# Kernel optimization log

Measured on AMD Instinct MI355X. Metric: run time of the kernel, lower is better.

## Reference

```python
import jax, jax.numpy as jnp
import numpy as np

DIM = 1024; DEPTH = 6; HEADS = 16; DH = 64; NF = 16; VOCAB = 20000; B = 4; N = 1024
INNER = HEADS * DH
FF_INNER = int(DIM * 4 * 2 / 3)  # GEGLU inner dim = 2730


def _ln(x, g):
    # torch F.layer_norm with beta=0 buffer, eps=1e-5
    m = x.mean(-1, keepdims=True)
    v = ((x - m) ** 2).mean(-1, keepdims=True)
    return (x - m) / jnp.sqrt(v + 1e-5) * g


def _attn(x, ctx, mask, ln_g, Wq, Wkv, Wo):
    # faithful: LayerNorm applied to x (queries); context, if given, used raw for k/v
    xn = _ln(x, ln_g)
    kv_x = xn if ctx is None else ctx
    b, i, _ = x.shape
    j = kv_x.shape[1]
    q = (xn @ Wq).reshape(b, i, HEADS, DH) * (DH ** -0.5)
    k, v = jnp.split(kv_x @ Wkv, 2, axis=-1)
    k = k.reshape(b, j, HEADS, DH)
    v = v.reshape(b, j, HEADS, DH)
    sim = jnp.einsum('bihd,bjhd->bhij', q, k)
    sim = jnp.where(mask, sim, -jnp.finfo(sim.dtype).max)
    attn = jax.nn.softmax(sim, axis=-1)
    out = jnp.einsum('bhij,bjhd->bihd', attn, v).reshape(b, i, INNER)
    return out @ Wo


def _closs(a, b, ls):
    # CLIP-style ContrastiveLossWithTemperature
    an = a / jnp.linalg.norm(a, axis=-1, keepdims=True)
    bn = b / jnp.linalg.norm(b, axis=-1, keepdims=True)
    logits = jnp.exp(ls) * (an @ bn.T)
    lab = jnp.arange(a.shape[0])
    la = -jax.nn.log_softmax(logits, axis=-1)[lab, lab].mean()
    lb = -jax.nn.log_softmax(logits.T, axis=-1)[lab, lab].mean()
    return (la + lb) * 0.5


def setup_inputs() -> dict:
    key = jax.random.key(0)
    ks = jax.random.split(key, 16)
    rn = lambda k, s: jax.random.normal(k, s, jnp.float32) * 0.02
    return {
        'spliced_data': jax.random.normal(ks[0], (B, N), jnp.float32),
        'spliced_index': jax.random.randint(ks[1], (B, N), 0, VOCAB),
        'emb': rn(ks[2], (VOCAB, DIM)),
        'fusion_tokens': jax.random.normal(ks[3], (NF, DIM), jnp.float32),
        'return_tokens': jax.random.normal(ks[4], (2, DIM), jnp.float32),
        'ln1_g': jnp.ones((DEPTH, DIM), jnp.float32),
        'Wq': rn(ks[5], (DEPTH, DIM, INNER)),
        'Wkv': rn(ks[6], (DEPTH, DIM, 2 * INNER)),
        'Wo': rn(ks[7], (DEPTH, INNER, DIM)),
        'ln2_g': jnp.ones((DEPTH, DIM), jnp.float32),
        'Wff1': rn(ks[8], (DEPTH, DIM, 2 * FF_INNER)),
        'Wff2': rn(ks[9], (DEPTH, FF_INNER, DIM)),
        'norm_g': jnp.ones((DIM,), jnp.float32),
        'pool_ln_g': jnp.ones((DIM,), jnp.float32),
        'pWq': rn(ks[10], (DIM, INNER)),
        'pWkv': rn(ks[11], (DIM, 2 * INNER)),
        'pWo': rn(ks[12], (INNER, DIM)),
        'logit_scale_c': jnp.float32(np.log(1.0 / 0.07)),
        'logit_scale_f': jnp.float32(np.log(1.0 / 0.07)),
    }


def reference(spliced_data, spliced_index, emb, fusion_tokens, return_tokens,
              ln1_g, Wq, Wkv, Wo, ln2_g, Wff1, Wff2, norm_g,
              pool_ln_g, pWq, pWkv, pWo, logit_scale_c, logit_scale_f):
    b = spliced_data.shape[0]
    # BioZorroEncoder: value-weighted embedding lookup
    spliced_tokens = emb[spliced_index] * spliced_data[..., None]  # [b, N, DIM]
    tokens = jnp.concatenate(
        [spliced_tokens, jnp.broadcast_to(fusion_tokens, (b, NF, DIM))], axis=1)
    tt = jnp.concatenate([jnp.zeros((N,), jnp.int32), jnp.ones((NF,), jnp.int32)])
    # spliced attends spliced; fusion attends everything
    zmask = (tt[:, None] == tt[None, :]) | (tt[:, None] == 1)

    def body(t, p):
        l1, wq, wkv, wo, l2, w1, w2 = p
        t = _attn(t, None, zmask, l1, wq, wkv, wo) + t
        h = _ln(t, l2) @ w1
        xh, gate = jnp.split(h, 2, axis=-1)
        t = (jax.nn.gelu(gate, approximate=False) * xh) @ w2 + t
        return t, None

    tokens, _ = jax.lax.scan(body, tokens, (ln1_g, Wq, Wkv, Wo, ln2_g, Wff1, Wff2))
    tokens = _ln(tokens, norm_g)

    rtt = jnp.array([0, 1], jnp.int32)
    pm0 = rtt[:, None] == tt[None, :]
    # faithful to source operator precedence: (pm0 | rtt) == GLOBAL(2) -> all False
    pm = (pm0.astype(jnp.int32) | rtt[:, None]) == 2

    ret = jnp.broadcast_to(return_tokens, (b, 2, DIM))
    pooled = _attn(ret, tokens, pm, pool_ln_g, pWq, pWkv, pWo) + ret

    spliced = pooled[:, 0]
    fusion = pooled[:, 1]
    loss = _closs(spliced, spliced, logit_scale_c) + _closs(spliced, fusion, logit_scale_f)
    return loss
```

## Files before the change

### kernel.cpp

```cpp
#include <hip/hip_runtime.h>

typedef unsigned short u16;
typedef unsigned long long u64;
typedef __attribute__((ext_vector_type(8))) short short8;
typedef __attribute__((ext_vector_type(4))) float f32x4;

__device__ __forceinline__ u16 f2b(float f) {
  union { float f; unsigned u; } x; x.f = f;
  unsigned r = x.u + 0x7fffu + ((x.u >> 16) & 1u);
  return (u16)(r >> 16);
}
__device__ __forceinline__ float b2f(u16 h) {
  union { unsigned u; float f; } x; x.u = ((unsigned)h) << 16;
  return x.f;
}
__device__ __forceinline__ void gld16(const void* g, void* l) {
  __builtin_amdgcn_global_load_lds(
      (__attribute__((address_space(1))) const void*)g,
      (__attribute__((address_space(3))) void*)l, 16, 0, 0);
}

__global__ __launch_bounds__(256) void embed_k(
    const float* __restrict__ data, const int* __restrict__ idx,
    const float* __restrict__ emb, const float* __restrict__ fus,
    float* __restrict__ t) {
  int row = blockIdx.x;
  int b = row / 1040, n = row % 1040;
  int tid = threadIdx.x;
  const float4* src;
  float sc = 1.f;
  if (n < 1024) {
    int e = idx[b * 1024 + n];
    sc = data[b * 1024 + n];
    src = (const float4*)(emb + (long)e * 1024);
  } else {
    src = (const float4*)(fus + (long)(n - 1024) * 1024);
  }
  float4 v = src[tid];
  v.x *= sc; v.y *= sc; v.z *= sc; v.w *= sc;
  ((float4*)(t + (long)row * 1024))[tid] = v;
}

__global__ __launch_bounds__(256) void wtrans5_k(
    const float* __restrict__ sWq, const float* __restrict__ sWkv,
    const float* __restrict__ sWo, const float* __restrict__ sW1,
    const float* __restrict__ sW2,
    u16* __restrict__ dQkvT, u16* __restrict__ dWoT,
    u16* __restrict__ dF1T, u16* __restrict__ dF2T) {
  int id = blockIdx.x;
  const float* src; u16* dst; int K, N, Kpad, nx; float sc = 1.f;
  if (id < 1024)       { src = sWq;  dst = dQkvT;             K = 1024; N = 1024; Kpad = 1024; nx = 32; sc = 0.125f; }
  else if (id < 3072)  { id -= 1024; src = sWkv; dst = dQkvT + 1024 * 1024; K = 1024; N = 2048; Kpad = 1024; nx = 64; }
  else if (id < 4096)  { id -= 3072; src = sWo;  dst = dWoT;  K = 1024; N = 1024; Kpad = 1024; nx = 32; }
  else if (id < 9600)  { id -= 4096; src = sW1;  dst = dF1T;  K = 1024; N = 5460; Kpad = 1024; nx = 172; }
  else                 { id -= 9600; src = sW2;  dst = dF2T;  K = 2730; N = 1024; Kpad = 2752; nx = 32; }
  int n0 = (id % nx) * 32, k0 = (id / nx) * 32;
  __shared__ float tile[32][33];
  int x = threadIdx.x & 31, y = threadIdx.x >> 5;
#pragma unroll
  for (int i = 0; i < 4; i++) {
    int k = k0 + y + i * 8, n = n0 + x;
    tile[y + i * 8][x] = (k < K && n < N) ? src[(long)k * N + n] * sc : 0.f;
  }
  __syncthreads();
#pragma unroll
  for (int i = 0; i < 4; i++) {
    int n = n0 + y + i * 8, k = k0 + x;
    dst[(long)n * Kpad + k] = f2b(tile[x][y + i * 8]);
  }
}

__global__ __launch_bounds__(256) void ln_k(
    const float* __restrict__ t, const float* __restrict__ g,
    u16* __restrict__ xn) {
  int row = blockIdx.x, tid = threadIdx.x;
  int wave = tid >> 6, lane = tid & 63;
  float4 v = ((const float4*)(t + (long)row * 1024))[tid];
  float s = v.x + v.y + v.z + v.w;
#pragma unroll
  for (int o = 32; o > 0; o >>= 1) s += __shfl_xor(s, o, 64);
  __shared__ float r1[4], r2[4];
  if (lane == 0) r1[wave] = s;
  __syncthreads();
  float mean = (r1[0] + r1[1] + r1[2] + r1[3]) * (1.f / 1024.f);
  float dx = v.x - mean, dy = v.y - mean, dz = v.z - mean, dw = v.w - mean;
  float q = dx * dx + dy * dy + dz * dz + dw * dw;
#pragma unroll
  for (int o = 32; o > 0; o >>= 1) q += __shfl_xor(q, o, 64);
  if (lane == 0) r2[wave] = q;
  __syncthreads();
  float var = (r2[0] + r2[1] + r2[2] + r2[3]) * (1.f / 1024.f);
  float inv = rsqrtf(var + 1e-5f);
  float4 gv = ((const float4*)g)[tid];
  u64 pack = (u64)f2b(dx * inv * gv.x)
           | ((u64)f2b(dy * inv * gv.y) << 16)
           | ((u64)f2b(dz * inv * gv.z) << 32)
           | ((u64)f2b(dw * inv * gv.w) << 48);
  *(u64*)(xn + (long)row * 1024 + tid * 4) = pack;
}

__global__ __launch_bounds__(256) void lnred_k(
    float* __restrict__ t, const float* __restrict__ p0, const float* __restrict__ p1,
    const float* __restrict__ g, u16* __restrict__ xn) {
  int row = blockIdx.x, tid = threadIdx.x;
  int wave = tid >> 6, lane = tid & 63;
  long base = (long)row * 1024;
  float4 v = ((const float4*)(t + base))[tid];
  float4 a = ((const float4*)(p0 + base))[tid];
  float4 bq = ((const float4*)(p1 + base))[tid];
  v.x += a.x + bq.x; v.y += a.y + bq.y; v.z += a.z + bq.z; v.w += a.w + bq.w;
  ((float4*)(t + base))[tid] = v;
  float s = v.x + v.y + v.z + v.w;
#pragma unroll
  for (int o = 32; o > 0; o >>= 1) s += __shfl_xor(s, o, 64);
  __shared__ float r1[4], r2[4];
  if (lane == 0) r1[wave] = s;
  __syncthreads();
  float mean = (r1[0] + r1[1] + r1[2] + r1[3]) * (1.f / 1024.f);
  float dx = v.x - mean, dy = v.y - mean, dz = v.z - mean, dw = v.w - mean;
  float q = dx * dx + dy * dy + dz * dz + dw * dw;
#pragma unroll
  for (int o = 32; o > 0; o >>= 1) q += __shfl_xor(q, o, 64);
  if (lane == 0) r2[wave] = q;
  __syncthreads();
  float var = (r2[0] + r2[1] + r2[2] + r2[3]) * (1.f / 1024.f);
  float inv = rsqrtf(var + 1e-5f);
  float4 gv = ((const float4*)g)[tid];
  u64 pack = (u64)f2b(dx * inv * gv.x)
           | ((u64)f2b(dy * inv * gv.y) << 16)
           | ((u64)f2b(dz * inv * gv.z) << 32)
           | ((u64)f2b(dw * inv * gv.w) << 48);
  *(u64*)(xn + base + tid * 4) = pack;
}

__global__ __launch_bounds__(256) void redrow_k(
    float* __restrict__ t, const float* __restrict__ p0, const float* __restrict__ p1,
    float* __restrict__ rowm, float* __restrict__ rinv) {
  int row = blockIdx.x, tid = threadIdx.x;
  int wave = tid >> 6, lane = tid & 63;
  long base = (long)row * 1024;
  float4 v = ((const float4*)(t + base))[tid];
  float4 a = ((const float4*)(p0 + base))[tid];
  float4 bq = ((const float4*)(p1 + base))[tid];
  v.x += a.x + bq.x; v.y += a.y + bq.y; v.z += a.z + bq.z; v.w += a.w + bq.w;
  ((float4*)(t + base))[tid] = v;
  float s = v.x + v.y + v.z + v.w;
#pragma unroll
  for (int o = 32; o > 0; o >>= 1) s += __shfl_xor(s, o, 64);
  __shared__ float r1[4], r2[4];
  if (lane == 0) r1[wave] = s;
  __syncthreads();
  float mean = (r1[0] + r1[1] + r1[2] + r1[3]) * (1.f / 1024.f);
  float dx = v.x - mean, dy = v.y - mean, dz = v.z - mean, dw = v.w - mean;
  float q = dx * dx + dy * dy + dz * dz + dw * dw;
#pragma unroll
  for (int o = 32; o > 0; o >>= 1) q += __shfl_xor(q, o, 64);
  if (lane == 0) r2[wave] = q;
  __syncthreads();
  if (tid == 0) {
    float var = (r2[0] + r2[1] + r2[2] + r2[3]) * (1.f / 1024.f);
    rowm[row] = mean;
    rinv[row] = rsqrtf(var + 1e-5f);
  }
}

__global__ __launch_bounds__(256) void gemm_bt(
    const u16* __restrict__ A, int lda,
    const u16* __restrict__ Bt, int ldb,
    void* __restrict__ C, int ldc,
    int K, int mode, int gx, int ns, long pstride) {
  __shared__ u16 As[3][128 * 32];
  __shared__ u16 Bs[3][128 * 32];
  int tid = threadIdx.x;
  int wave = tid >> 6, lane = tid & 63;
  int col = lane & 15, grp = lane >> 4;
  int nwg = gridDim.x;
  int id = blockIdx.x;
  int q = nwg >> 3, r = nwg & 7;
  int xcd = id & 7, off = id >> 3;
  int wgid = (xcd < r ? xcd * (q + 1) : r * (q + 1) + (xcd - r) * q) + off;
  int tiles = nwg / ns;
  int ksp = wgid / tiles;
  int rem = wgid % tiles;
  int bm = rem % gx, bn = rem / gx;
  int nst = K >> 5;
  int k0 = ((nst * ksp) / ns) << 5;
  int k1 = ((nst * (ksp + 1)) / ns) << 5;
  int sr = wave * 16 + (lane >> 2);
  int sk = ((lane & 3) ^ ((lane >> 3) & 3)) * 8;
  const u16* aSrc = A + ((long)bm * 128 + sr) * lda + sk;
  const u16* bSrc = Bt + ((long)bn * 128 + sr) * ldb + sk;
  int wm = (wave >> 1) * 64, wn = (wave & 1) * 64;
  f32x4 acc[4][4] = {};

#define GSTAGE(buf, kt) do { \
    _Pragma("unroll") \
    for (int qq = 0; qq < 2; qq++) { \
      gld16(aSrc + (kt) + (long)qq * 64 * lda, &As[buf][wave * 512 + qq * 2048]); \
      gld16(bSrc + (kt) + (long)qq * 64 * ldb, &Bs[buf][wave * 512 + qq * 2048]); \
    } } while (0)

  GSTAGE(0, k0);
  if (k0 + 32 < k1) GSTAGE(1, k0 + 32);
  int cur = 0;
  int slot = (grp ^ ((col >> 1) & 3)) * 8;
  for (int kt = k0; kt < k1; kt += 32) {
    if (kt + 64 < k1) {
      int nb = cur + 2; if (nb >= 3) nb -= 3;
      GSTAGE(nb, kt + 64);
      asm volatile("s_waitcnt vmcnt(8)" ::: "memory");
    } else if (kt + 32 < k1) {
      asm volatile("s_waitcnt vmcnt(4)" ::: "memory");
    } else {
      asm volatile("s_waitcnt vmcnt(0)" ::: "memory");
    }
    __builtin_amdgcn_s_barrier();
    __builtin_amdgcn_sched_barrier(0);
    short8 af[4], bfv[4];
#pragma unroll
    for (int m = 0; m < 4; m++)
      af[m] = *(const short8*)&As[cur][(wm + m * 16 + col) * 32 + slot];
#pragma unroll
    for (int n = 0; n < 4; n++)
      bfv[n] = *(const short8*)&Bs[cur][(wn + n * 16 + col) * 32 + slot];
    __builtin_amdgcn_s_setprio(1);
#pragma unroll
    for (int m = 0; m < 4; m++)
#pragma unroll
      for (int n = 0; n < 4; n++)
        acc[m][n] = __builtin_amdgcn_mfma_f32_16x16x32_bf16(af[m], bfv[n], acc[m][n], 0, 0, 0);
    __builtin_amdgcn_s_setprio(0);
    __builtin_amdgcn_s_barrier();
    __builtin_amdgcn_sched_barrier(0);
    cur = (cur == 2) ? 0 : cur + 1;
  }
#undef GSTAGE
  long r0 = (long)bm * 128 + wm + grp * 4;
  int c0 = bn * 128 + wn + col;
  if (mode == 0) {
    u16* Cb = (u16*)C;
#pragma unroll
    for (int m = 0; m < 4; m++)
#pragma unroll
      for (int n = 0; n < 4; n++)
#pragma unroll
        for (int rr = 0; rr < 4; rr++)
          Cb[(r0 + m * 16 + rr) * ldc + c0 + n * 16] = f2b(acc[m][n][rr]);
  } else {
    float* Cf = (float*)C + (long)ksp * pstride;
#pragma unroll
    for (int m = 0; m < 4; m++)
#pragma unroll
      for (int n = 0; n < 4; n++)
#pragma unroll
        for (int rr = 0; rr < 4; rr++)
          Cf[(r0 + m * 16 + rr) * ldc + c0 + n * 16] = acc[m][n][rr];
  }
}

__global__ __launch_bounds__(256) void vtrans_k(
    const u16* __restrict__ qkv, u16* __restrict__ vt) {
  int bh = blockIdx.x, jt = blockIdx.y;
  int b = bh >> 4, h = bh & 15;
  __shared__ u16 tile[64][65];
  int x = threadIdx.x & 63, y = threadIdx.x >> 6;
#pragma unroll
  for (int r = 0; r < 16; r++) {
    int jl = r * 4 + y;
    int j = jt * 64 + jl;
    u16 val = 0;
    if (j < 1040) val = qkv[((long)b * 1040 + j) * 3072 + 2048 + h * 64 + x];
    tile[jl][x] = val;
  }
  __syncthreads();
  long ob = (long)bh * 64 * 1040;
#pragma unroll
  for (int r = 0; r < 16; r++) {
    int d = r * 4 + y;
    int j = jt * 64 + x;
    if (j < 1040) vt[ob + (long)d * 1040 + j] = tile[x][d];
  }
}

__global__ __launch_bounds__(256) void attn_k(
    const u16* __restrict__ qkv, const u16* __restrict__ vt,
    u16* __restrict__ out) {
  int bh = blockIdx.x, it = blockIdx.y;
  int b = bh >> 4, h = bh & 15;
  int tid = threadIdx.x, wave = tid >> 6, lane = tid & 63;
  int col = lane & 15, grp = lane >> 4;
  int i0 = it * 64;
  int jmax = (it == 16) ? 1040 : 1024;
  const u16* qb = qkv + (long)b * 1040 * 3072 + h * 64;
  const u16* kb = qkv + (long)b * 1040 * 3072 + 1024 + h * 64;
  const u16* vb = vt + (long)bh * 64 * 1040;
  __shared__ u16 Ks[2][64 * 64];
  __shared__ u16 Vs[2][64 * 64];
  __shared__ u16 Ps[4][16 * 64];

  int srow0 = wave * 8 + (lane >> 3);
  int gsw = ((lane & 7) ^ (srow0 & 7)) * 8;
#define ASTAGE(buf, j0s) do { \
    _Pragma("unroll") \
    for (int qq = 0; qq < 2; qq++) { \
      int rr = qq * 32 + srow0; \
      gld16(kb + (long)((j0s) + rr) * 3072 + gsw, &Ks[buf][qq * 2048 + wave * 512]); \
      gld16(vb + (long)rr * 1040 + (j0s) + gsw, &Vs[buf][qq * 2048 + wave * 512]); \
    } } while (0)

  short8 aq[2];
  int qrow = i0 + wave * 16;
#pragma unroll
  for (int kf = 0; kf < 2; kf++)
    aq[kf] = *(const short8*)(qb + (long)(qrow + col) * 3072 + kf * 32 + grp * 8);

  f32x4 oa[4] = {};
  float lrow[4] = {0.f, 0.f, 0.f, 0.f};

  ASTAGE(0, 0);
  int cur = 0;
  for (int j0 = 0; j0 < jmax; j0 += 64) {
    if (j0 + 64 < jmax) {
      ASTAGE(cur ^ 1, j0 + 64);
      asm volatile("s_waitcnt vmcnt(4)" ::: "memory");
    } else {
      asm volatile("s_waitcnt vmcnt(0)" ::: "memory");
    }
    __builtin_amdgcn_s_barrier();
    __builtin_amdgcn_sched_barrier(0);
    f32x4 s[4] = {};
#pragma unroll
    for (int kf = 0; kf < 2; kf++) {
      short8 bk[4];
#pragma unroll
      for (int n = 0; n < 4; n++) {
        int rk = n * 16 + col;
        bk[n] = *(const short8*)&Ks[cur][rk * 64 + ((kf * 32 + grp * 8) ^ ((rk & 7) << 3))];
      }
      __builtin_amdgcn_s_setprio(1);
#pragma unroll
      for (int n = 0; n < 4; n++)
        s[n] = __builtin_amdgcn_mfma_f32_16x16x32_bf16(aq[kf], bk[n], s[n], 0, 0, 0);
      __builtin_amdgcn_s_setprio(0);
    }
    if (j0 + 64 > jmax) {
      int lim = jmax - j0;
#pragma unroll
      for (int n = 0; n < 4; n++) {
        if (n * 16 + col >= lim) {
#pragma unroll
          for (int r = 0; r < 4; r++) s[n][r] = -1e30f;
        }
      }
    }
#pragma unroll
    for (int r = 0; r < 4; r++) {
      int rp = grp * 4 + r;
      float rs = 0.f;
#pragma unroll
      for (int n = 0; n < 4; n++) {
        float p = __expf(s[n][r]);
        rs += p;
        Ps[wave][rp * 64 + ((n * 16 + col) ^ ((rp & 7) << 3))] = f2b(p);
      }
#pragma unroll
      for (int o = 1; o < 16; o <<= 1) rs += __shfl_xor(rs, o, 64);
      lrow[r] += rs;
    }
#pragma unroll
    for (int kf = 0; kf < 2; kf++) {
      short8 ap, bv[4];
      int rm = col;
      ap = *(const short8*)&Ps[wave][rm * 64 + ((kf * 32 + grp * 8) ^ ((rm & 7) << 3))];
#pragma unroll
      for (int n = 0; n < 4; n++) {
        int rv = n * 16 + col;
        bv[n] = *(const short8*)&Vs[cur][rv * 64 + ((kf * 32 + grp * 8) ^ ((rv & 7) << 3))];
      }
      __builtin_amdgcn_s_setprio(1);
#pragma unroll
      for (int n = 0; n < 4; n++)
        oa[n] = __builtin_amdgcn_mfma_f32_16x16x32_bf16(ap, bv[n], oa[n], 0, 0, 0);
      __builtin_amdgcn_s_setprio(0);
    }
    __builtin_amdgcn_s_barrier();
    __builtin_amdgcn_sched_barrier(0);
    cur ^= 1;
  }
#undef ASTAGE
#pragma unroll
  for (int n = 0; n < 4; n++)
#pragma unroll
    for (int r = 0; r < 4; r++) {
      int i = i0 + wave * 16 + grp * 4 + r;
      if (i < 1040)
        out[((long)b * 1040 + i) * 1024 + h * 64 + n * 16 + col] = f2b(oa[n][r] / lrow[r]);
    }
}

__global__ __launch_bounds__(256) void act_k(
    const u16* __restrict__ h, u16* __restrict__ act) {
  int row = blockIdx.x;
  int c = blockIdx.y * 1024 + threadIdx.x * 4;
  if (c >= 2752) return;
  const u16* hr = h + (long)row * 5504;
  u64 pack = 0;
#pragma unroll
  for (int i = 0; i < 4; i++) {
    int cc = c + i;
    float r = 0.f;
    if (cc < 2730) {
      float xh = b2f(hr[cc]);
      float gt = b2f(hr[2730 + cc]);
      float ge = 0.5f * gt * (1.f + erff(gt * 0.70710678118f));
      r = ge * xh;
    }
    pack |= ((u64)f2b(r)) << (16 * i);
  }
  *(u64*)(act + (long)row * 2752 + c) = pack;
}

__global__ __launch_bounds__(256) void wcolsum_k(
    const float* __restrict__ t, const float* __restrict__ rowm,
    const float* __restrict__ rinv, float* __restrict__ colsum,
    float* __restrict__ msum) {
  int b = blockIdx.x, c = blockIdx.y, tid = threadIdx.x;
  float a0 = 0, a1 = 0, a2 = 0, a3 = 0, ms = 0;
  for (int r = 0; r < 20; r++) {
    long row = (long)b * 1040 + c * 20 + r;
    float iv = rinv[row];
    float4 v = ((const float4*)(t + row * 1024))[tid];
    a0 += v.x * iv; a1 += v.y * iv; a2 += v.z * iv; a3 += v.w * iv;
    if (tid == 0) ms += rowm[row] * iv;
  }
  atomicAdd(&colsum[b * 1024 + tid * 4 + 0], a0);
  atomicAdd(&colsum[b * 1024 + tid * 4 + 1], a1);
  atomicAdd(&colsum[b * 1024 + tid * 4 + 2], a2);
  atomicAdd(&colsum[b * 1024 + tid * 4 + 3], a3);
  if (tid == 0) atomicAdd(&msum[b], ms);
}

__global__ __launch_bounds__(256) void mv1_k(
    const float* __restrict__ colsum, const float* __restrict__ msum,
    const float* __restrict__ g, const float* __restrict__ pWkv,
    float* __restrict__ tmp) {
  int b = blockIdx.x, n = blockIdx.y * 256 + threadIdx.x;
  float msb = msum[b];
  float acc = 0.f;
  for (int k = 0; k < 1024; k++) {
    float mk = g[k] * (colsum[b * 1024 + k] - msb);
    acc += mk * pWkv[(long)k * 2048 + 1024 + n];
  }
  tmp[b * 1024 + n] = acc * (1.f / 1040.f);
}

__global__ __launch_bounds__(256) void mv2_k(
    const float* __restrict__ tmp, const float* __restrict__ pWo,
    const float* __restrict__ ret, float* __restrict__ spl,
    float* __restrict__ fub) {
  int b = blockIdx.x, n = blockIdx.y * 256 + threadIdx.x;
  float acc = 0.f;
  for (int k = 0; k < 1024; k++) acc += tmp[b * 1024 + k] * pWo[(long)k * 1024 + n];
  spl[b * 1024 + n] = ret[n] + acc;
  fub[b * 1024 + n] = ret[1024 + n] + acc;
}

__device__ float closs_dev(const float L[4][4]) {
  float la = 0.f, lb = 0.f;
  for (int i = 0; i < 4; i++) {
    float mx = fmaxf(fmaxf(L[i][0], L[i][1]), fmaxf(L[i][2], L[i][3]));
    float sm = expf(L[i][0] - mx) + expf(L[i][1] - mx) + expf(L[i][2] - mx) + expf(L[i][3] - mx);
    la += mx + logf(sm) - L[i][i];
  }
  for (int j = 0; j < 4; j++) {
    float mx = fmaxf(fmaxf(L[0][j], L[1][j]), fmaxf(L[2][j], L[3][j]));
    float sm = expf(L[0][j] - mx) + expf(L[1][j] - mx) + expf(L[2][j] - mx) + expf(L[3][j] - mx);
    lb += mx + logf(sm) - L[j][j];
  }
  return 0.125f * (la + lb);
}

__global__ __launch_bounds__(256) void loss_k(
    const float* __restrict__ s, const float* __restrict__ f,
    const float* __restrict__ lsc, const float* __restrict__ lsf,
    float* __restrict__ out) {
  __shared__ float dots[36];
  int tid = threadIdx.x, wave = tid >> 6, lane = tid & 63;
  for (int d = wave; d < 36; d += 4) {
    const float *a, *bb;
    if (d < 16) { a = s + (d >> 2) * 1024; bb = s + (d & 3) * 1024; }
    else if (d < 32) { int e = d - 16; a = s + (e >> 2) * 1024; bb = f + (e & 3) * 1024; }
    else { a = f + (d - 32) * 1024; bb = a; }
    float p = 0.f;
    for (int k = lane; k < 1024; k += 64) p += a[k] * bb[k];
#pragma unroll
    for (int o = 32; o > 0; o >>= 1) p += __shfl_xor(p, o, 64);
    if (lane == 0) dots[d] = p;
  }
  __syncthreads();
  if (tid == 0) {
    float nS[4], nF[4];
    for (int i = 0; i < 4; i++) { nS[i] = sqrtf(dots[i * 4 + i]); nF[i] = sqrtf(dots[32 + i]); }
    float e1 = expf(lsc[0]), e2 = expf(lsf[0]);
    float L1[4][4], L2[4][4];
    for (int i = 0; i < 4; i++)
      for (int j = 0; j < 4; j++) {
        L1[i][j] = e1 * dots[i * 4 + j] / (nS[i] * nS[j]);
        L2[i][j] = e2 * dots[16 + i * 4 + j] / (nS[i] * nF[j]);
      }
    out[0] = closs_dev(L1) + closs_dev(L2);
  }
}

extern "C" void kernel_launch(void* const* d_in, const int* in_sizes, int n_in,
                              void* d_out, int out_size, void* d_ws, size_t ws_size,
                              hipStream_t stream) {
  (void)in_sizes; (void)n_in; (void)out_size; (void)ws_size;
  const float* sdata = (const float*)d_in[0];
  const int*   sidx  = (const int*)d_in[1];
  const float* emb   = (const float*)d_in[2];
  const float* fus   = (const float*)d_in[3];
  const float* ret   = (const float*)d_in[4];
  const float* ln1g  = (const float*)d_in[5];
  const float* Wq    = (const float*)d_in[6];
  const float* Wkv   = (const float*)d_in[7];
  const float* Wo    = (const float*)d_in[8];
  const float* ln2g  = (const float*)d_in[9];
  const float* Wff1  = (const float*)d_in[10];
  const float* Wff2  = (const float*)d_in[11];
  const float* normg = (const float*)d_in[12];
  const float* pWkv  = (const float*)d_in[15];
  const float* pWo   = (const float*)d_in[16];
  const float* lsc   = (const float*)d_in[17];
  const float* lsf   = (const float*)d_in[18];

  char* ws = (char*)d_ws;
  float* t   = (float*)(ws + 0L);
  u16* xn    = (u16*)(ws + 17301504L);
  char* U    = ws + 25952256L;
  u16* qkv   = (u16*)(U);
  u16* vtb   = (u16*)(U + 26738688L);
  u16* aout  = (u16*)(U + 35270656L);
  u16* hb    = (u16*)(U);
  u16* ab    = (u16*)(U + 46497792L);
  float* par0 = (float*)(U);
  float* par1 = (float*)(U + 17301504L);
  char* WT   = ws + 95698944L;
  u16* qkvT  = (u16*)(WT);
  u16* WoT   = (u16*)(WT + 6291456L);
  u16* f1T   = (u16*)(WT + 8388608L);
  u16* f2T   = (u16*)(WT + 19660800L);
  char* FIN  = ws + 120995840L;
  float* rowm   = (float*)(FIN);
  float* rinvp  = (float*)(FIN + 16640L);
  float* colsum = (float*)(FIN + 33280L);
  float* msum   = (float*)(FIN + 49664L);
  float* tmp    = (float*)(FIN + 49728L);
  float* spl    = (float*)(FIN + 66112L);
  float* fub    = (float*)(FIN + 82496L);
  const long PSTR = 4224L * 1024;

  embed_k<<<4160, 256, 0, stream>>>(sdata, sidx, emb, fus, t);

  for (int l = 0; l < 6; l++) {
    wtrans5_k<<<12352, 256, 0, stream>>>(
        Wq + (long)l * 1024 * 1024, Wkv + (long)l * 1024 * 2048,
        Wo + (long)l * 1024 * 1024, Wff1 + (long)l * 1024 * 5460,
        Wff2 + (long)l * 2730 * 1024, qkvT, WoT, f1T, f2T);

    if (l == 0)
      ln_k<<<4160, 256, 0, stream>>>(t, ln1g, xn);
    else
      lnred_k<<<4160, 256, 0, stream>>>(t, par0, par1, ln1g + l * 1024, xn);

    gemm_bt<<<33 * 24, 256, 0, stream>>>(xn, 1024, qkvT, 1024, qkv, 3072, 1024, 0, 33, 1, 0);
    vtrans_k<<<dim3(64, 17), 256, 0, stream>>>(qkv, vtb);
    attn_k<<<dim3(64, 17), 256, 0, stream>>>(qkv, vtb, aout);
    gemm_bt<<<33 * 8 * 2, 256, 0, stream>>>(aout, 1024, WoT, 1024, par0, 1024, 1024, 1, 33, 2, PSTR);
    lnred_k<<<4160, 256, 0, stream>>>(t, par0, par1, ln2g + l * 1024, xn);
    gemm_bt<<<33 * 43, 256, 0, stream>>>(xn, 1024, f1T, 1024, hb, 5504, 1024, 0, 33, 1, 0);
    act_k<<<dim3(4160, 3), 256, 0, stream>>>(hb, ab);
    gemm_bt<<<33 * 8 * 2, 256, 0, stream>>>(ab, 2752, f2T, 2752, par0, 1024, 2752, 1, 33, 2, PSTR);
  }

  redrow_k<<<4160, 256, 0, stream>>>(t, par0, par1, rowm, rinvp);
  hipMemsetAsync(colsum, 0, 16448, stream);
  wcolsum_k<<<dim3(4, 52), 256, 0, stream>>>(t, rowm, rinvp, colsum, msum);
  mv1_k<<<dim3(4, 4), 256, 0, stream>>>(colsum, msum, normg, pWkv, tmp);
  mv2_k<<<dim3(4, 4), 256, 0, stream>>>(tmp, pWo, ret, spl, fub);
  loss_k<<<1, 256, 0, stream>>>(spl, fub, lsc, lsf, (float*)d_out);
}
```

Baseline: 2.074 ms.

## Fuse V transpose into QKV GEMM epilogue and compute softmax row sums via MFMA

The QKV GEMM gains a mode that, for V-column tiles, also writes the transposed V layout straight from the accumulators, so the separate vtrans kernel launch and its extra read and write of V go away. The attention kernel clamps V tile loads at the sequence end, because the padded region is no longer zero-filled. It also computes the softmax row sums with an extra MFMA against a ones vector, dropping the per-row shuffle reductions. The risks are strided 8-byte scattered stores in the GEMM epilogue, and row sums now taken from bf16-rounded probabilities.

```diff
diff --git a/kernel.cpp b/kernel.cpp
--- a/kernel.cpp
+++ b/kernel.cpp
@@ -168,7 +168,7 @@
     const u16* __restrict__ A, int lda,
     const u16* __restrict__ Bt, int ldb,
     void* __restrict__ C, int ldc,
-    int K, int mode, int gx, int ns, long pstride) {
+    int K, int mode, int gx, int ns, long pstride, u16* __restrict__ vt) {
   __shared__ u16 As[3][128 * 32];
   __shared__ u16 Bs[3][128 * 32];
   int tid = threadIdx.x;
@@ -237,7 +237,7 @@
 #undef GSTAGE
   long r0 = (long)bm * 128 + wm + grp * 4;
   int c0 = bn * 128 + wn + col;
-  if (mode == 0) {
+  if (mode != 1) {
     u16* Cb = (u16*)C;
 #pragma unroll
     for (int m = 0; m < 4; m++)
@@ -246,6 +246,25 @@
 #pragma unroll
         for (int rr = 0; rr < 4; rr++)
           Cb[(r0 + m * 16 + rr) * ldc + c0 + n * 16] = f2b(acc[m][n][rr]);
+    if (mode == 2 && bn >= 16) {
+#pragma unroll
+      for (int m = 0; m < 4; m++) {
+        long row = r0 + m * 16;
+        if (row < 4160) {
+          int bidx = (int)(row / 1040);
+          int j = (int)(row - (long)bidx * 1040);
+#pragma unroll
+          for (int n = 0; n < 4; n++) {
+            int d = c0 + n * 16 - 2048;
+            u64 pack = (u64)f2b(acc[m][n][0])
+                     | ((u64)f2b(acc[m][n][1]) << 16)
+                     | ((u64)f2b(acc[m][n][2]) << 32)
+                     | ((u64)f2b(acc[m][n][3]) << 48);
+            *(u64*)(vt + ((long)(bidx * 16 + (d >> 6)) * 64 + (d & 63)) * 1040 + j) = pack;
+          }
+        }
+      }
+    }
   } else {
     float* Cf = (float*)C + (long)ksp * pstride;
 #pragma unroll
@@ -255,30 +274,6 @@
 #pragma unroll
         for (int rr = 0; rr < 4; rr++)
           Cf[(r0 + m * 16 + rr) * ldc + c0 + n * 16] = acc[m][n][rr];
-  }
-}
-
-__global__ __launch_bounds__(256) void vtrans_k(
-    const u16* __restrict__ qkv, u16* __restrict__ vt) {
-  int bh = blockIdx.x, jt = blockIdx.y;
-  int b = bh >> 4, h = bh & 15;
-  __shared__ u16 tile[64][65];
-  int x = threadIdx.x & 63, y = threadIdx.x >> 6;
-#pragma unroll
-  for (int r = 0; r < 16; r++) {
-    int jl = r * 4 + y;
-    int j = jt * 64 + jl;
-    u16 val = 0;
-    if (j < 1040) val = qkv[((long)b * 1040 + j) * 3072 + 2048 + h * 64 + x];
-    tile[jl][x] = val;
-  }
-  __syncthreads();
-  long ob = (long)bh * 64 * 1040;
-#pragma unroll
-  for (int r = 0; r < 16; r++) {
-    int d = r * 4 + y;
-    int j = jt * 64 + x;
-    if (j < 1040) vt[ob + (long)d * 1040 + j] = tile[x][d];
   }
 }
 
@@ -301,11 +296,12 @@
   int srow0 = wave * 8 + (lane >> 3);
   int gsw = ((lane & 7) ^ (srow0 & 7)) * 8;
 #define ASTAGE(buf, j0s) do { \
+    int jv = (j0s) + gsw; if (jv >= 1040) jv = 1032; \
     _Pragma("unroll") \
     for (int qq = 0; qq < 2; qq++) { \
       int rr = qq * 32 + srow0; \
       gld16(kb + (long)((j0s) + rr) * 3072 + gsw, &Ks[buf][qq * 2048 + wave * 512]); \
-      gld16(vb + (long)rr * 1040 + (j0s) + gsw, &Vs[buf][qq * 2048 + wave * 512]); \
+      gld16(vb + (long)rr * 1040 + jv, &Vs[buf][qq * 2048 + wave * 512]); \
     } } while (0)
 
   short8 aq[2];
@@ -314,8 +310,14 @@
   for (int kf = 0; kf < 2; kf++)
     aq[kf] = *(const short8*)(qb + (long)(qrow + col) * 3072 + kf * 32 + grp * 8);
 
+  short8 one8 = {};
+  if (col == 0) {
+#pragma unroll
+    for (int i = 0; i < 8; i++) one8[i] = (short)0x3F80;
+  }
+
   f32x4 oa[4] = {};
-  float lrow[4] = {0.f, 0.f, 0.f, 0.f};
+  f32x4 oa1 = {};
 
   ASTAGE(0, 0);
   int cur = 0;
@@ -356,16 +358,11 @@
 #pragma unroll
     for (int r = 0; r < 4; r++) {
       int rp = grp * 4 + r;
-      float rs = 0.f;
 #pragma unroll
       for (int n = 0; n < 4; n++) {
         float p = __expf(s[n][r]);
-        rs += p;
         Ps[wave][rp * 64 + ((n * 16 + col) ^ ((rp & 7) << 3))] = f2b(p);
       }
-#pragma unroll
-      for (int o = 1; o < 16; o <<= 1) rs += __shfl_xor(rs, o, 64);
-      lrow[r] += rs;
     }
 #pragma unroll
     for (int kf = 0; kf < 2; kf++) {
@@ -381,6 +378,7 @@
 #pragma unroll
       for (int n = 0; n < 4; n++)
         oa[n] = __builtin_amdgcn_mfma_f32_16x16x32_bf16(ap, bv[n], oa[n], 0, 0, 0);
+      oa1 = __builtin_amdgcn_mfma_f32_16x16x32_bf16(ap, one8, oa1, 0, 0, 0);
       __builtin_amdgcn_s_setprio(0);
     }
     __builtin_amdgcn_s_barrier();
@@ -388,13 +386,16 @@
     cur ^= 1;
   }
 #undef ASTAGE
+  float lr[4];
+#pragma unroll
+  for (int r = 0; r < 4; r++) lr[r] = __shfl(oa1[r], lane & 48, 64);
 #pragma unroll
   for (int n = 0; n < 4; n++)
 #pragma unroll
     for (int r = 0; r < 4; r++) {
       int i = i0 + wave * 16 + grp * 4 + r;
       if (i < 1040)
-        out[((long)b * 1040 + i) * 1024 + h * 64 + n * 16 + col] = f2b(oa[n][r] / lrow[r]);
+        out[((long)b * 1040 + i) * 1024 + h * 64 + n * 16 + col] = f2b(oa[n][r] / lr[r]);
     }
 }
 
@@ -573,14 +574,13 @@
     else
       lnred_k<<<4160, 256, 0, stream>>>(t, par0, par1, ln1g + l * 1024, xn);
 
-    gemm_bt<<<33 * 24, 256, 0, stream>>>(xn, 1024, qkvT, 1024, qkv, 3072, 1024, 0, 33, 1, 0);
-    vtrans_k<<<dim3(64, 17), 256, 0, stream>>>(qkv, vtb);
+    gemm_bt<<<33 * 24, 256, 0, stream>>>(xn, 1024, qkvT, 1024, qkv, 3072, 1024, 2, 33, 1, 0, vtb);
     attn_k<<<dim3(64, 17), 256, 0, stream>>>(qkv, vtb, aout);
-    gemm_bt<<<33 * 8 * 2, 256, 0, stream>>>(aout, 1024, WoT, 1024, par0, 1024, 1024, 1, 33, 2, PSTR);
+    gemm_bt<<<33 * 8 * 2, 256, 0, stream>>>(aout, 1024, WoT, 1024, par0, 1024, 1024, 1, 33, 2, PSTR, vtb);
     lnred_k<<<4160, 256, 0, stream>>>(t, par0, par1, ln2g + l * 1024, xn);
-    gemm_bt<<<33 * 43, 256, 0, stream>>>(xn, 1024, f1T, 1024, hb, 5504, 1024, 0, 33, 1, 0);
+    gemm_bt<<<33 * 43, 256, 0, stream>>>(xn, 1024, f1T, 1024, hb, 5504, 1024, 0, 33, 1, 0, vtb);
     act_k<<<dim3(4160, 3), 256, 0, stream>>>(hb, ab);
-    gemm_bt<<<33 * 8 * 2, 256, 0, stream>>>(ab, 2752, f2T, 2752, par0, 1024, 2752, 1, 33, 2, PSTR);
+    gemm_bt<<<33 * 8 * 2, 256, 0, stream>>>(ab, 2752, f2T, 2752, par0, 1024, 2752, 1, 33, 2, PSTR, vtb);
   }
 
   redrow_k<<<4160, 256, 0, stream>>>(t, par0, par1, rowm, rinvp);
```

Measured after the change: 1.993 ms. 3.9% less time.
